# Optimization experiments

Measured on AMD Instinct MI355X. Metric: run time of the kernel, lower is better.

## Reference

```python
import jax, jax.numpy as jnp
import numpy as np

B = 65536
D = 512            # resnet18 fc.in_features
NUM_CLASSES = 512  # size of batch_centers
LEVELS = [2048, 1024, 512]


def setup_inputs() -> dict:
    key = jax.random.key(0)
    ks = jax.random.split(key, 8)
    x = jax.random.normal(ks[0], (B, D), dtype=jnp.float32)
    labels = jax.random.randint(ks[1], (B,), 0, NUM_CLASSES, dtype=jnp.int64)
    W0 = jax.random.normal(ks[2], (LEVELS[0], D), dtype=jnp.float32) * 0.02
    b0 = jnp.zeros((LEVELS[0],), dtype=jnp.float32)
    W1 = jax.random.normal(ks[3], (LEVELS[1], LEVELS[0]), dtype=jnp.float32) * 0.02
    b1 = jnp.zeros((LEVELS[1],), dtype=jnp.float32)
    W2 = jax.random.normal(ks[4], (LEVELS[2], LEVELS[1]), dtype=jnp.float32) * 0.02
    b2 = jnp.zeros((LEVELS[2],), dtype=jnp.float32)
    lambda_values = jnp.array([1e-3, 1.0, 1.0, 1.0], dtype=jnp.float32)
    return {"x": x, "W0": W0, "b0": b0, "W1": W1, "b1": b1,
            "W2": W2, "b2": b2, "lambda_values": lambda_values,
            "labels": labels}


def _cross_entropy(logits, labels):
    # mean over batch of -log p(label) (torch CrossEntropyLoss default)
    logp = jax.nn.log_softmax(logits, axis=-1)
    nll = -jnp.take_along_axis(logp, labels[:, None], axis=-1)[:, 0]
    return jnp.mean(nll)


def reference(x, W0, b0, W1, b1, W2, b2, lambda_values, labels):
    # --- per-class scatter-mean centers (vectorized segment reduce) ---
    sums = jax.ops.segment_sum(x, labels, num_segments=NUM_CLASSES)
    counts = jax.ops.segment_sum(jnp.ones((x.shape[0],), x.dtype), labels,
                                 num_segments=NUM_CLASSES)
    centers = jnp.where(counts[:, None] > 0,
                        sums / jnp.maximum(counts, 1.0)[:, None],
                        0.0)  # classes absent from batch keep zero centers
    # --- gather-diff center loss: sum_i ||x_i - c_{y_i}||^2 ---
    diff = x - centers[labels]
    center_loss = jnp.sum(diff * diff)
    # --- cascaded classification heads, CE at each level ---
    h = x
    losses = []
    for W, b in ((W0, b0), (W1, b1), (W2, b2)):
        h = h @ W.T + b
        losses.append(_cross_entropy(h, labels))
    classification_losses = jnp.stack(losses)
    return lambda_values[0] * center_loss + jnp.dot(lambda_values[1:],
                                                    classification_losses)
```

## Files before the change

kernel.cpp:

```cpp
#include <hip/hip_runtime.h>
#include <cstdint>
#include <cstddef>

using f32x4  = __attribute__((ext_vector_type(4))) float;
using i32x4v = __attribute__((ext_vector_type(4))) int;
using i32x8v = __attribute__((ext_vector_type(8))) int;

__device__ __forceinline__ unsigned char f2fp8(float f) {
  return (unsigned char)(__builtin_amdgcn_cvt_pk_fp8_f32(f, f, 0, false) & 0xff);
}

__device__ __forceinline__ float fp8b0(unsigned int w) {
  return __builtin_amdgcn_cvt_f32_fp8(w, 0);
}
__device__ __forceinline__ float fp8b1(unsigned int w) {
  return __builtin_amdgcn_cvt_f32_fp8(w, 1);
}
__device__ __forceinline__ float fp8b2(unsigned int w) {
  return __builtin_amdgcn_cvt_f32_fp8(w, 2);
}
__device__ __forceinline__ float fp8b3(unsigned int w) {
  return __builtin_amdgcn_cvt_f32_fp8(w, 3);
}

__device__ __forceinline__ float waveRed(float v) {
#pragma unroll
  for (int m = 32; m >= 1; m >>= 1) v += __shfl_xor(v, m, 64);
  return v;
}

__device__ __forceinline__ void gload16(const void* g, void* l) {
  __builtin_amdgcn_global_load_lds(
      (__attribute__((address_space(1))) uint32_t*)(uintptr_t)g,
      (__attribute__((address_space(3))) uint32_t*)(uint32_t*)l,
      16, 0, 0);
}

__device__ __forceinline__ i32x8v cvt32(const float* p) {
  const float4* p4 = (const float4*)p;
  int d0, d1, d2, d3, d4, d5, d6, d7;
#define CVT1(N)                                                      \
  {                                                                  \
    const float4 f = p4[N];                                          \
    int w_ = __builtin_amdgcn_cvt_pk_fp8_f32(f.x, f.y, 0, false);    \
    w_ = __builtin_amdgcn_cvt_pk_fp8_f32(f.z, f.w, w_, true);        \
    d##N = w_;                                                       \
  }
  CVT1(0) CVT1(1) CVT1(2) CVT1(3) CVT1(4) CVT1(5) CVT1(6) CVT1(7)
#undef CVT1
  return (i32x8v){d0, d1, d2, d3, d4, d5, d6, d7};
}

__device__ __forceinline__ i32x8v ldfrag(const unsigned char* bb, int off) {
  const i32x4v lo = *(const i32x4v*)(bb + off);
  const i32x4v hi = *(const i32x4v*)(bb + off + 1024);
  return (i32x8v){lo[0], lo[1], lo[2], lo[3], hi[0], hi[1], hi[2], hi[3]};
}

__global__ __launch_bounds__(256) void prep_w(
    const float4* __restrict__ W1, const float4* __restrict__ W2,
    const float4* __restrict__ W0f4, const float* __restrict__ W0,
    const float* __restrict__ b0,
    uint32_t* __restrict__ W1_8, uint32_t* __restrict__ W2_8,
    uint32_t* __restrict__ W0_8, unsigned char* __restrict__ W0t8,
    float* __restrict__ zr, int zwords, float* __restrict__ biascat) {
  __shared__ unsigned char t8[64][65];
  const int b = blockIdx.x;
  const int tid = threadIdx.x;
  if (b < 1024) {
    for (int i = b * 256 + tid; i < 524288; i += 1024 * 256) {
      float4 v = W1[i];
      int p = __builtin_amdgcn_cvt_pk_fp8_f32(v.x, v.y, 0, false);
      p = __builtin_amdgcn_cvt_pk_fp8_f32(v.z, v.w, p, true);
      W1_8[i] = (uint32_t)p;
    }
  } else if (b < 1280) {
    for (int i = (b - 1024) * 256 + tid; i < 131072; i += 256 * 256) {
      float4 v = W2[i];
      int p = __builtin_amdgcn_cvt_pk_fp8_f32(v.x, v.y, 0, false);
      p = __builtin_amdgcn_cvt_pk_fp8_f32(v.z, v.w, p, true);
      W2_8[i] = (uint32_t)p;
    }
  } else if (b < 1536) {
    for (int i = (b - 1280) * 256 + tid; i < 262144; i += 256 * 256) {
      float4 v = W0f4[i];
      int p = __builtin_amdgcn_cvt_pk_fp8_f32(v.x, v.y, 0, false);
      p = __builtin_amdgcn_cvt_pk_fp8_f32(v.z, v.w, p, true);
      W0_8[i] = (uint32_t)p;
    }
  } else if (b < 1792) {
    const int t = b - 1536;
    const int r0 = (t >> 3) * 64, c0 = (t & 7) * 64;
#pragma unroll
    for (int p = 0; p < 16; ++p) {
      const int row = p * 4 + (tid >> 6), col = tid & 63;
      t8[row][col] = f2fp8(W0[(size_t)(r0 + row) * 512 + c0 + col]);
    }
    __syncthreads();
#pragma unroll
    for (int p = 0; p < 16; ++p) {
      const int oc = p * 4 + (tid >> 6), orr = tid & 63;
      W0t8[(size_t)(c0 + oc) * 2048 + r0 + orr] = t8[orr][oc];
    }
  } else {
    const int zb = (zwords + 255) >> 8;
    if (b < 1792 + zb) {
      const int i = (b - 1792) * 256 + tid;
      if (i < zwords) zr[i] = 0.f;
    } else {
      const int i = (b - 1792 - zb) * 256 + tid;
      if (i < 2048) biascat[i] = b0[i];
    }
  }
}

__global__ __launch_bounds__(256) void count_k(const int* __restrict__ lab,
                                               int* __restrict__ counts, int n) {
  __shared__ int h[512];
  for (int i = threadIdx.x; i < 512; i += 256) h[i] = 0;
  __syncthreads();
  for (int i = blockIdx.x * 256 + threadIdx.x; i < n; i += gridDim.x * 256)
    atomicAdd(&h[lab[i]], 1);
  __syncthreads();
  for (int i = threadIdx.x; i < 512; i += 256) {
    int v = h[i];
    if (v) atomicAdd(&counts[i], v);
  }
}

__global__ void prefix_k(const int* __restrict__ counts, int* __restrict__ offsets,
                         int* __restrict__ cursor, int nc) {
  const int lane = threadIdx.x;
  int base = 0;
  for (int c0 = 0; c0 < nc; c0 += 64) {
    int v = counts[c0 + lane];
    int x = v;
#pragma unroll
    for (int d = 1; d < 64; d <<= 1) {
      int y = __shfl_up(x, d, 64);
      if (lane >= d) x += y;
    }
    int excl = base + x - v;
    offsets[c0 + lane] = excl;
    cursor[c0 + lane] = excl;
    base += __shfl(x, 63, 64);
  }
}

__global__ void scatter_k(const int* __restrict__ lab, int* __restrict__ cursor,
                          int* __restrict__ buckets, int n) {
  for (int i = blockIdx.x * 256 + threadIdx.x; i < n; i += gridDim.x * 256) {
    int pos = atomicAdd(&cursor[lab[i]], 1);
    buckets[pos] = i;
  }
}

__global__ __launch_bounds__(256) void csum_k(const float* __restrict__ x,
    const int* __restrict__ buckets, const int* __restrict__ offsets,
    const int* __restrict__ counts, float* __restrict__ centers4,
    float* __restrict__ scal) {
  const int c = blockIdx.x >> 2, q = blockIdx.x & 3;
  const int cnt = counts[c];
  const int t = threadIdx.x;
  float sx = 0.f, sy = 0.f, ssq = 0.f;
  if (cnt) {
    const int beg = offsets[c];
    const int lo = beg + (cnt * q) / 4, hi = beg + (cnt * (q + 1)) / 4;
    for (int i = lo; i < hi; ++i) {
      const int row = buckets[i];
      const float2 v = ((const float2*)(x + (size_t)row * 512))[t];
      sx += v.x;
      sy += v.y;
      ssq += v.x * v.x + v.y * v.y;
    }
  }
  float2* dst = (float2*)(centers4 + (size_t)((c << 2) + q) * 512);
  dst[t] = make_float2(sx, sy);
  ssq = waveRed(ssq);
  __shared__ float red[4];
  if ((t & 63) == 0) red[t >> 6] = ssq;
  __syncthreads();
  if (t == 0) {
    const float s = red[0] + red[1] + red[2] + red[3];
    if (s != 0.f) atomicAdd(&scal[0], s);
  }
}

__global__ __launch_bounds__(256) void cnorm_k(const float* __restrict__ centers4,
    float* __restrict__ centers, const int* __restrict__ counts,
    float* __restrict__ out) {
  const int c = blockIdx.x;
  const int t = threadIdx.x;
  const float2* p = (const float2*)(centers4 + (size_t)(c << 2) * 512);
  float2 s = p[t];
  float2 s1 = p[t + 256], s2 = p[t + 512], s3 = p[t + 768];
  s.x += s1.x + s2.x + s3.x;
  s.y += s1.y + s2.y + s3.y;
  ((float2*)(centers + (size_t)c * 512))[t] = s;
  const int cnt = counts[c];
  if (cnt == 0) return;
  float ssq = s.x * s.x + s.y * s.y;
  ssq = waveRed(ssq);
  __shared__ float red[4];
  if ((t & 63) == 0) red[t >> 6] = ssq;
  __syncthreads();
  if (t == 0)
    atomicAdd(out, (red[0] + red[1] + red[2] + red[3]) / (float)cnt);
}

__global__ __launch_bounds__(256) void matvec_k(const float* __restrict__ W,
    const float* __restrict__ vin, const float* __restrict__ badd,
    float* __restrict__ vout, int K) {
  int row = blockIdx.x;
  float s = 0.f;
  for (int k = threadIdx.x; k < K; k += 256) s += W[(size_t)row * K + k] * vin[k];
  s = waveRed(s);
  __shared__ float red[4];
  if ((threadIdx.x & 63) == 0) red[threadIdx.x >> 6] = s;
  __syncthreads();
  if (threadIdx.x == 0) vout[row] = red[0] + red[1] + red[2] + red[3] + badd[row];
}

__global__ void pk_k(const float* __restrict__ centers,
                     const unsigned char* __restrict__ Bcat8,
                     const float* __restrict__ biascat,
                     const int* __restrict__ counts, float* __restrict__ scal) {
  const int b = blockIdx.x;
  const int lvl = b >> 9;
  const int c = b & 511;
  const int lane = threadIdx.x;
  const int cbase = (lvl == 0) ? 0 : (lvl == 1) ? 2048 : 3072;
  const float4* S = (const float4*)(centers + (size_t)c * 512);
  const uint2 wb = ((const uint2*)(Bcat8 + (size_t)(cbase + c) * 512))[lane];
  const float4 s0 = S[lane * 2];
  const float4 s1 = S[lane * 2 + 1];
  float s = s0.x * fp8b0(wb.x) + s0.y * fp8b1(wb.x) +
            s0.z * fp8b2(wb.x) + s0.w * fp8b3(wb.x) +
            s1.x * fp8b0(wb.y) + s1.y * fp8b1(wb.y) +
            s1.z * fp8b2(wb.y) + s1.w * fp8b3(wb.y);
  s = waveRed(s);
  if (lane == 0)
    atomicAdd(&scal[5 + lvl], s + (float)counts[c] * biascat[cbase + c]);
}

__global__ __launch_bounds__(256) void gemm8_w(
    const unsigned char* __restrict__ A8, const unsigned char* __restrict__ B8,
    int M, int N, int K, unsigned char* __restrict__ C8,
    unsigned char* __restrict__ Ct8) {
  __shared__ __align__(16) unsigned char As[128 * 128];
  __shared__ __align__(16) unsigned char Bs[128 * 128];
  const int tid = threadIdx.x;
  const int lane = tid & 63;
  const int wave = tid >> 6;
  const int lane16 = lane & 15;
  const int quad = lane >> 4;
  const int wm = (wave >> 1) * 64;
  const int wn = (wave & 1) * 64;
  const int m0 = blockIdx.y * 128;
  const int n0 = blockIdx.x * 128;

  f32x4 acc[4][4] = {};

  int srow[4], goff[4];
#pragma unroll
  for (int q = 0; q < 4; ++q) {
    const int s = tid + q * 256;
    const int row = s >> 3;
    const int c16 = s & 7;
    srow[q] = row;
    goff[q] = (((c16 >> 1) ^ (row & 3)) << 5) + ((c16 & 1) << 4);
  }

  for (int kt = 0; kt < K; kt += 128) {
#pragma unroll
    for (int q = 0; q < 4; ++q) {
      const int s = tid + q * 256;
      gload16(A8 + (size_t)(m0 + srow[q]) * K + kt + goff[q], &As[s * 16]);
      gload16(B8 + (size_t)(n0 + srow[q]) * K + kt + goff[q], &Bs[s * 16]);
    }
    __syncthreads();
    i32x8v a8[4], b8[4];
#pragma unroll
    for (int i = 0; i < 4; ++i) {
      const int row = i * 16 + lane16;
      const int sc = quad ^ (row & 3);
      const unsigned char* pa = &As[row * 128 + sc * 32];
      const i32x4v lo = *(const i32x4v*)pa;
      const i32x4v hi = *(const i32x4v*)(pa + 16);
      a8[i] = (i32x8v){lo[0], lo[1], lo[2], lo[3], hi[0], hi[1], hi[2], hi[3]};
    }
#pragma unroll
    for (int j = 0; j < 4; ++j) {
      const int row = j * 16 + lane16;
      const int sc = quad ^ (row & 3);
      const unsigned char* pb = &Bs[row * 128 + sc * 32];
      const i32x4v lo = *(const i32x4v*)pb;
      const i32x4v hi = *(const i32x4v*)(pb + 16);
      b8[j] = (i32x8v){lo[0], lo[1], lo[2], lo[3], hi[0], hi[1], hi[2], hi[3]};
    }
#pragma unroll
    for (int i = 0; i < 4; ++i)
#pragma unroll
      for (int j = 0; j < 4; ++j)
        acc[i][j] = __builtin_amdgcn_mfma_scale_f32_16x16x128_f8f6f4(
            a8[i], b8[j], acc[i][j], 0, 0, 0, 0x7f7f7f7f, 0, 0x7f7f7f7f);
    __syncthreads();
  }
#pragma unroll
  for (int i = 0; i < 4; ++i)
#pragma unroll
    for (int r = 0; r < 4; ++r) {
      const int rowg = m0 + wm + i * 16 + quad * 4 + r;
#pragma unroll
      for (int j = 0; j < 4; ++j) {
        const int colg = n0 + wn + j * 16 + lane16;
        const unsigned char v8 = f2fp8(acc[i][j][r]);
        C8[(size_t)rowg * N + colg] = v8;
        if (Ct8) Ct8[(size_t)colg * M + rowg] = v8;
      }
    }
}

__global__ void reorder_k(const unsigned char* __restrict__ in,
                          unsigned char* __restrict__ out) {
  const int id = blockIdx.x * 256 + threadIdx.x;
  const int col = id >> 4;
  const int k32 = id & 15;
  const int kt = k32 >> 2, quad = k32 & 3;
  const int l = quad * 16 + (col & 15);
  const size_t src = (size_t)col * 512 + k32 * 32;
  const size_t fragbase = (size_t)(col >> 6) * 32768 + (size_t)kt * 8192 +
                          (size_t)((col >> 4) & 3) * 2048;
  const uint4 a = *(const uint4*)(in + src);
  const uint4 b = *(const uint4*)(in + src + 16);
  *(uint4*)(out + fragbase + l * 16) = a;
  *(uint4*)(out + fragbase + 1024 + l * 16) = b;
}

__global__ __launch_bounds__(256, 1) void gemm_ce8(
    const float* __restrict__ x, const unsigned char* __restrict__ Bp,
    const float* __restrict__ bias, float* __restrict__ scal) {
  __shared__ __align__(16) unsigned char Bl[4][8192];
  __shared__ float biasl[3584];
  const int tid = threadIdx.x;
  const int lane = tid & 63;
  const int wave = tid >> 6;
  const int lane16 = lane & 15;
  const int quad = lane >> 4;
  const int m0 = blockIdx.x * 256 + wave * 64;

  for (int i = tid; i < 3584; i += 256) biasl[i] = bias[i];

  i32x8v a[4][4];
#pragma unroll
  for (int i = 0; i < 4; ++i) {
    const float* xr = x + (size_t)(m0 + i * 16 + lane16) * 512 + quad * 32;
#pragma unroll
    for (int kt = 0; kt < 4; ++kt) a[i][kt] = cvt32(xr + kt * 128);
  }
  __syncthreads();

  const int soff = wave * 2048 + lane * 16;
  const unsigned char* bsrc = Bp + soff;
#pragma unroll
  for (int c = 0; c < 3; ++c) {
    gload16(bsrc, &Bl[c][soff]);
    gload16(bsrc + 1024, &Bl[c][soff + 1024]);
    bsrc += 8192;
  }
  int sc = 3;
  asm volatile("s_waitcnt vmcnt(4)" ::: "memory");
  __builtin_amdgcn_s_barrier();

  const int l16 = lane * 16;
  float es[16];
#pragma unroll
  for (int k = 0; k < 16; ++k) es[k] = 0.f;

#define MFMA4(KS, BF, J)                                                      \
  acc[0][J] = __builtin_amdgcn_mfma_scale_f32_16x16x128_f8f6f4(               \
      a[0][KS], BF, acc[0][J], 0, 0, 0, 0x7f7f7f7f, 0, 0x7f7f7f7f);           \
  acc[1][J] = __builtin_amdgcn_mfma_scale_f32_16x16x128_f8f6f4(               \
      a[1][KS], BF, acc[1][J], 0, 0, 0, 0x7f7f7f7f, 0, 0x7f7f7f7f);           \
  acc[2][J] = __builtin_amdgcn_mfma_scale_f32_16x16x128_f8f6f4(               \
      a[2][KS], BF, acc[2][J], 0, 0, 0, 0x7f7f7f7f, 0, 0x7f7f7f7f);           \
  acc[3][J] = __builtin_amdgcn_mfma_scale_f32_16x16x128_f8f6f4(               \
      a[3][KS], BF, acc[3][J], 0, 0, 0, 0x7f7f7f7f, 0, 0x7f7f7f7f);

#define KSTEP(KS)                                                             \
  {                                                                           \
    gload16(bsrc, &Bl[(KS + 3) & 3][soff]);                                   \
    gload16(bsrc + 1024, &Bl[(KS + 3) & 3][soff + 1024]);                     \
    bsrc += 8192;                                                             \
    if (++sc == 224) { sc = 0; bsrc = Bp + soff; }                            \
    i32x8v bf0 = ldfrag(&Bl[KS][0], l16);                                     \
    i32x8v bf1 = ldfrag(&Bl[KS][0], 2048 + l16);                              \
    asm volatile("s_waitcnt lgkmcnt(2)" ::: "memory");                        \
    __builtin_amdgcn_sched_barrier(0);                                        \
    __builtin_amdgcn_s_setprio(1);                                            \
    MFMA4(KS, bf0, 0)                                                         \
    i32x8v bf2 = ldfrag(&Bl[KS][0], 4096 + l16);                              \
    asm volatile("s_waitcnt lgkmcnt(2)" ::: "memory");                        \
    __builtin_amdgcn_sched_barrier(0);                                        \
    MFMA4(KS, bf1, 1)                                                         \
    i32x8v bf3 = ldfrag(&Bl[KS][0], 6144 + l16);                              \
    asm volatile("s_waitcnt lgkmcnt(2)" ::: "memory");                        \
    __builtin_amdgcn_sched_barrier(0);                                        \
    MFMA4(KS, bf2, 2)                                                         \
    asm volatile("s_waitcnt lgkmcnt(0)" ::: "memory");                        \
    __builtin_amdgcn_sched_barrier(0);                                        \
    MFMA4(KS, bf3, 3)                                                         \
    __builtin_amdgcn_s_setprio(0);                                            \
    asm volatile("s_waitcnt vmcnt(4)" ::: "memory");                          \
    __builtin_amdgcn_s_barrier();                                             \
  }

  int tile = 0;
#pragma unroll 1
  for (int lvl = 0; lvl < 3; ++lvl) {
    const int nt = (lvl == 0) ? 32 : (lvl == 1) ? 16 : 8;
#pragma unroll 1
    for (int t = 0; t < nt; ++t, ++tile) {
      f32x4 acc[4][4] = {};
      KSTEP(0)
      KSTEP(1)
      KSTEP(2)
      KSTEP(3)
      const float bj0 = biasl[tile * 64 + lane16];
      const float bj1 = biasl[tile * 64 + 16 + lane16];
      const float bj2 = biasl[tile * 64 + 32 + lane16];
      const float bj3 = biasl[tile * 64 + 48 + lane16];
#pragma unroll
      for (int i = 0; i < 4; ++i)
#pragma unroll
        for (int r = 0; r < 4; ++r)
          es[i * 4 + r] += __expf(acc[i][0][r] + bj0) +
                           __expf(acc[i][1][r] + bj1) +
                           __expf(acc[i][2][r] + bj2) +
                           __expf(acc[i][3][r] + bj3);
    }
    float ls = 0.f;
#pragma unroll
    for (int k = 0; k < 16; ++k) {
      float tot = es[k];
      tot += __shfl_xor(tot, 1, 64);
      tot += __shfl_xor(tot, 2, 64);
      tot += __shfl_xor(tot, 4, 64);
      tot += __shfl_xor(tot, 8, 64);
      if (lane16 == 0) ls += __logf(tot);
      es[k] = 0.f;
    }
    ls = waveRed(ls);
    if (lane == 0) atomicAdd(&scal[2 + lvl], ls);
  }
#undef KSTEP
#undef MFMA4
}

__global__ void fin_k(const float* __restrict__ scal, const float* __restrict__ lam,
                      float* __restrict__ out, float invB) {
  if (threadIdx.x == 0 && blockIdx.x == 0)
    out[0] = lam[0] * (scal[0] - scal[1]) +
             (lam[1] * (scal[2] - scal[5]) + lam[2] * (scal[3] - scal[6]) +
              lam[3] * (scal[4] - scal[7])) * invB;
}

extern "C" void kernel_launch(void* const* d_in, const int* in_sizes, int n_in,
                              void* d_out, int out_size, void* d_ws, size_t ws_size,
                              hipStream_t stream) {
  const float* x   = (const float*)d_in[0];
  const float* W0  = (const float*)d_in[1];
  const float* b0  = (const float*)d_in[2];
  const float* W1  = (const float*)d_in[3];
  const float* b1  = (const float*)d_in[4];
  const float* W2  = (const float*)d_in[5];
  const float* b2  = (const float*)d_in[6];
  const float* lam = (const float*)d_in[7];
  const int*   lab = (const int*)d_in[8];

  const int Bsz = in_sizes[8];
  const int D   = in_sizes[0] / Bsz;
  const int N0  = in_sizes[2];
  const int N1  = in_sizes[4];
  const int N2  = in_sizes[6];
  const int Ncat = N0 + N1 + N2;
  const int NCLS = 512;

  char* w = (char*)d_ws;
  size_t off = 0;
  auto alloc = [&](size_t bytes) -> void* {
    void* p = w + off;
    off += (bytes + 255) & ~(size_t)255;
    return p;
  };

  unsigned char* Bcat8 = (unsigned char*)alloc((size_t)Ncat * D);
  unsigned char* Bp    = (unsigned char*)alloc((size_t)Ncat * D + 16384);
  unsigned char* W1_8  = (unsigned char*)alloc((size_t)N1 * N0);
  unsigned char* W2_8  = (unsigned char*)alloc((size_t)N2 * N1);
  unsigned char* W0t8  = (unsigned char*)alloc((size_t)D * N0);
  unsigned char* M1t8  = (unsigned char*)alloc((size_t)D * N1);
  float* biascat  = (float*)alloc((size_t)Ncat * 4);
  int* offsets = (int*)alloc(NCLS * 4);
  int* cursor  = (int*)alloc(NCLS * 4);
  int* buckets = (int*)alloc((size_t)Bsz * 4);
  float* centers4 = (float*)alloc((size_t)NCLS * 512 * 4 * 4);
  float* centers  = (float*)alloc((size_t)NCLS * 512 * 4);
  const int zwords = NCLS + 8;
  char* zr = (char*)alloc((size_t)zwords * 4);
  int*   counts  = (int*)zr;
  float* scal    = (float*)(zr + NCLS * 4);
  (void)ws_size; (void)n_in; (void)out_size;

  const int zb = (zwords + 255) / 256;
  prep_w<<<dim3(1792 + zb + 8), dim3(256), 0, stream>>>(
      (const float4*)W1, (const float4*)W2, (const float4*)W0, W0, b0,
      (uint32_t*)W1_8, (uint32_t*)W2_8, (uint32_t*)Bcat8, W0t8,
      (float*)zr, zwords, biascat);

  count_k<<<dim3(32), dim3(256), 0, stream>>>(lab, counts, Bsz);
  prefix_k<<<dim3(1), dim3(64), 0, stream>>>(counts, offsets, cursor, NCLS);
  scatter_k<<<dim3(256), dim3(256), 0, stream>>>(lab, cursor, buckets, Bsz);
  csum_k<<<dim3(4 * NCLS), dim3(256), 0, stream>>>(x, buckets, offsets, counts,
                                                   centers4, scal);
  cnorm_k<<<dim3(NCLS), dim3(256), 0, stream>>>(centers4, centers, counts,
                                                &scal[1]);

  matvec_k<<<dim3(N1), dim3(256), 0, stream>>>(W1, b0, b1, biascat + N0, N0);
  matvec_k<<<dim3(N2), dim3(256), 0, stream>>>(W2, biascat + N0, b2, biascat + N0 + N1, N1);

  gemm8_w<<<dim3(D / 128, N1 / 128), dim3(256), 0, stream>>>(
      W1_8, W0t8, N1, D, N0, Bcat8 + (size_t)N0 * D, M1t8);
  gemm8_w<<<dim3(D / 128, N2 / 128), dim3(256), 0, stream>>>(
      W2_8, M1t8, N2, D, N1, Bcat8 + (size_t)(N0 + N1) * D, nullptr);

  reorder_k<<<dim3(Ncat * D / 32 / 256), dim3(256), 0, stream>>>(Bcat8, Bp);

  pk_k<<<dim3(3 * NCLS), dim3(64), 0, stream>>>(centers, Bcat8, biascat,
                                                counts, scal);

  gemm_ce8<<<dim3(Bsz / 256), dim3(256), 0, stream>>>(x, Bp, biascat, scal);

  fin_k<<<dim3(1), dim3(64), 0, stream>>>(scal, lam, (float*)d_out, 1.f / (float)Bsz);
}
```

Before: 563.0 us.

## Shrink gemm_ce8 row tile to 16 per wave and raise occupancy

Each wave now handles 16 rows instead of 64, so the A operand fits in four fragments and only four accumulators are live. The grid grows fourfold and launch bounds allow four blocks per CU, aiming to hide memory and barrier latency through more resident waves. The LDS bias copy and the interleaved waitcnt/setprio scheduling are removed, and bias is read straight from global memory. In exchange, each staged B tile is reused by a quarter as many rows, so global/L2 traffic for B and LDS fragment reads per MFMA both rise roughly fourfold.

```diff
diff --git a/kernel.cpp b/kernel.cpp
--- a/kernel.cpp
+++ b/kernel.cpp
@@ -337,28 +337,22 @@
   *(uint4*)(out + fragbase + 1024 + l * 16) = b;
 }
 
-__global__ __launch_bounds__(256, 1) void gemm_ce8(
+__global__ __launch_bounds__(256, 4) void gemm_ce8(
     const float* __restrict__ x, const unsigned char* __restrict__ Bp,
     const float* __restrict__ bias, float* __restrict__ scal) {
   __shared__ __align__(16) unsigned char Bl[4][8192];
-  __shared__ float biasl[3584];
   const int tid = threadIdx.x;
   const int lane = tid & 63;
   const int wave = tid >> 6;
   const int lane16 = lane & 15;
   const int quad = lane >> 4;
-  const int m0 = blockIdx.x * 256 + wave * 64;
-
-  for (int i = tid; i < 3584; i += 256) biasl[i] = bias[i];
-
-  i32x8v a[4][4];
-#pragma unroll
-  for (int i = 0; i < 4; ++i) {
-    const float* xr = x + (size_t)(m0 + i * 16 + lane16) * 512 + quad * 32;
-#pragma unroll
-    for (int kt = 0; kt < 4; ++kt) a[i][kt] = cvt32(xr + kt * 128);
-  }
-  __syncthreads();
+  const int m0 = blockIdx.x * 64 + wave * 16;
+
+  const float* xr = x + (size_t)(m0 + lane16) * 512 + quad * 32;
+  i32x8v a0 = cvt32(xr);
+  i32x8v a1 = cvt32(xr + 128);
+  i32x8v a2 = cvt32(xr + 256);
+  i32x8v a3 = cvt32(xr + 384);
 
   const int soff = wave * 2048 + lane * 16;
   const unsigned char* bsrc = Bp + soff;
@@ -373,44 +367,28 @@
   __builtin_amdgcn_s_barrier();
 
   const int l16 = lane * 16;
-  float es[16];
-#pragma unroll
-  for (int k = 0; k < 16; ++k) es[k] = 0.f;
-
-#define MFMA4(KS, BF, J)                                                      \
-  acc[0][J] = __builtin_amdgcn_mfma_scale_f32_16x16x128_f8f6f4(               \
-      a[0][KS], BF, acc[0][J], 0, 0, 0, 0x7f7f7f7f, 0, 0x7f7f7f7f);           \
-  acc[1][J] = __builtin_amdgcn_mfma_scale_f32_16x16x128_f8f6f4(               \
-      a[1][KS], BF, acc[1][J], 0, 0, 0, 0x7f7f7f7f, 0, 0x7f7f7f7f);           \
-  acc[2][J] = __builtin_amdgcn_mfma_scale_f32_16x16x128_f8f6f4(               \
-      a[2][KS], BF, acc[2][J], 0, 0, 0, 0x7f7f7f7f, 0, 0x7f7f7f7f);           \
-  acc[3][J] = __builtin_amdgcn_mfma_scale_f32_16x16x128_f8f6f4(               \
-      a[3][KS], BF, acc[3][J], 0, 0, 0, 0x7f7f7f7f, 0, 0x7f7f7f7f);
-
-#define KSTEP(KS)                                                             \
+  float es[4];
+#pragma unroll
+  for (int k = 0; k < 4; ++k) es[k] = 0.f;
+
+#define KSTEP(KS, AA)                                                         \
   {                                                                           \
     gload16(bsrc, &Bl[(KS + 3) & 3][soff]);                                   \
     gload16(bsrc + 1024, &Bl[(KS + 3) & 3][soff + 1024]);                     \
     bsrc += 8192;                                                             \
     if (++sc == 224) { sc = 0; bsrc = Bp + soff; }                            \
-    i32x8v bf0 = ldfrag(&Bl[KS][0], l16);                                     \
-    i32x8v bf1 = ldfrag(&Bl[KS][0], 2048 + l16);                              \
-    asm volatile("s_waitcnt lgkmcnt(2)" ::: "memory");                        \
-    __builtin_amdgcn_sched_barrier(0);                                        \
-    __builtin_amdgcn_s_setprio(1);                                            \
-    MFMA4(KS, bf0, 0)                                                         \
-    i32x8v bf2 = ldfrag(&Bl[KS][0], 4096 + l16);                              \
-    asm volatile("s_waitcnt lgkmcnt(2)" ::: "memory");                        \
-    __builtin_amdgcn_sched_barrier(0);                                        \
-    MFMA4(KS, bf1, 1)                                                         \
-    i32x8v bf3 = ldfrag(&Bl[KS][0], 6144 + l16);                              \
-    asm volatile("s_waitcnt lgkmcnt(2)" ::: "memory");                        \
-    __builtin_amdgcn_sched_barrier(0);                                        \
-    MFMA4(KS, bf2, 2)                                                         \
-    asm volatile("s_waitcnt lgkmcnt(0)" ::: "memory");                        \
-    __builtin_amdgcn_sched_barrier(0);                                        \
-    MFMA4(KS, bf3, 3)                                                         \
-    __builtin_amdgcn_s_setprio(0);                                            \
+    const i32x8v bf0 = ldfrag(&Bl[KS][0], l16);                               \
+    const i32x8v bf1 = ldfrag(&Bl[KS][0], 2048 + l16);                        \
+    const i32x8v bf2 = ldfrag(&Bl[KS][0], 4096 + l16);                        \
+    const i32x8v bf3 = ldfrag(&Bl[KS][0], 6144 + l16);                        \
+    acc0 = __builtin_amdgcn_mfma_scale_f32_16x16x128_f8f6f4(                  \
+        AA, bf0, acc0, 0, 0, 0, 0x7f7f7f7f, 0, 0x7f7f7f7f);                   \
+    acc1 = __builtin_amdgcn_mfma_scale_f32_16x16x128_f8f6f4(                  \
+        AA, bf1, acc1, 0, 0, 0, 0x7f7f7f7f, 0, 0x7f7f7f7f);                   \
+    acc2 = __builtin_amdgcn_mfma_scale_f32_16x16x128_f8f6f4(                  \
+        AA, bf2, acc2, 0, 0, 0, 0x7f7f7f7f, 0, 0x7f7f7f7f);                   \
+    acc3 = __builtin_amdgcn_mfma_scale_f32_16x16x128_f8f6f4(                  \
+        AA, bf3, acc3, 0, 0, 0, 0x7f7f7f7f, 0, 0x7f7f7f7f);                   \
     asm volatile("s_waitcnt vmcnt(4)" ::: "memory");                          \
     __builtin_amdgcn_s_barrier();                                             \
   }
@@ -421,27 +399,23 @@
     const int nt = (lvl == 0) ? 32 : (lvl == 1) ? 16 : 8;
 #pragma unroll 1
     for (int t = 0; t < nt; ++t, ++tile) {
-      f32x4 acc[4][4] = {};
-      KSTEP(0)
-      KSTEP(1)
-      KSTEP(2)
-      KSTEP(3)
-      const float bj0 = biasl[tile * 64 + lane16];
-      const float bj1 = biasl[tile * 64 + 16 + lane16];
-      const float bj2 = biasl[tile * 64 + 32 + lane16];
-      const float bj3 = biasl[tile * 64 + 48 + lane16];
-#pragma unroll
-      for (int i = 0; i < 4; ++i)
-#pragma unroll
-        for (int r = 0; r < 4; ++r)
-          es[i * 4 + r] += __expf(acc[i][0][r] + bj0) +
-                           __expf(acc[i][1][r] + bj1) +
-                           __expf(acc[i][2][r] + bj2) +
-                           __expf(acc[i][3][r] + bj3);
+      f32x4 acc0 = {}, acc1 = {}, acc2 = {}, acc3 = {};
+      KSTEP(0, a0)
+      KSTEP(1, a1)
+      KSTEP(2, a2)
+      KSTEP(3, a3)
+      const float bj0 = bias[tile * 64 + lane16];
+      const float bj1 = bias[tile * 64 + 16 + lane16];
+      const float bj2 = bias[tile * 64 + 32 + lane16];
+      const float bj3 = bias[tile * 64 + 48 + lane16];
+#pragma unroll
+      for (int r = 0; r < 4; ++r)
+        es[r] += __expf(acc0[r] + bj0) + __expf(acc1[r] + bj1) +
+                 __expf(acc2[r] + bj2) + __expf(acc3[r] + bj3);
     }
     float ls = 0.f;
 #pragma unroll
-    for (int k = 0; k < 16; ++k) {
+    for (int k = 0; k < 4; ++k) {
       float tot = es[k];
       tot += __shfl_xor(tot, 1, 64);
       tot += __shfl_xor(tot, 2, 64);
@@ -454,7 +428,6 @@
     if (lane == 0) atomicAdd(&scal[2 + lvl], ls);
   }
 #undef KSTEP
-#undef MFMA4
 }
 
 __global__ void fin_k(const float* __restrict__ scal, const float* __restrict__ lam,
@@ -539,7 +512,7 @@
   pk_k<<<dim3(3 * NCLS), dim3(64), 0, stream>>>(centers, Bcat8, biascat,
                                                 counts, scal);
 
-  gemm_ce8<<<dim3(Bsz / 256), dim3(256), 0, stream>>>(x, Bp, biascat, scal);
+  gemm_ce8<<<dim3(Bsz / 64), dim3(256), 0, stream>>>(x, Bp, biascat, scal);
 
   fin_k<<<dim3(1), dim3(64), 0, stream>>>(scal, lam, (float*)d_out, 1.f / (float)Bsz);
 }
```

Result: no change. 567.5 us (+0.8%).
